# Kernel tuning notes

Hardware: AMD Instinct MI355X
Metric: run time of the kernel (lower is better)

## Reference

```python
import jax, jax.numpy as jnp
import numpy as np

ALPHA_LO = float(np.exp(-1.0 / 5.0))   # 0.81873...
ALPHA_HI = float(np.exp(-1.0 / 25.0))  # 0.96079...
T_CROP = 0


def setup_inputs() -> dict:
    key = jax.random.key(0)
    k1, k2, k3, k4 = jax.random.split(key, 4)
    B, T, I, H = 64, 2000, 512, 512
    x = jax.random.normal(k1, (B, T, I), dtype=jnp.float32)
    # W ~ U(-sqrt(1/I), sqrt(1/I)) per nn.init.uniform_
    lim = float(np.sqrt(1.0 / I))
    W = jax.random.uniform(k2, (H, I), dtype=jnp.float32, minval=-lim, maxval=lim)
    # alpha ~ U(alpha_lim[0], alpha_lim[1])
    alpha = jax.random.uniform(k3, (H,), dtype=jnp.float32, minval=ALPHA_LO, maxval=ALPHA_HI)
    # initial membrane potential ~ U(0,1) (torch.rand in _readout_cell)
    u0 = jax.random.uniform(k4, (B, H), dtype=jnp.float32)
    return {"x": x, "W": W, "alpha": alpha, "u0": u0}


def reference(x, W, alpha, u0):
    # x: [B, T, I], W: [H, I] -> Wx: [B, T, H]
    alpha_c = jnp.clip(alpha, ALPHA_LO, ALPHA_HI)  # [H]
    beta = 1.0 - alpha_c                           # [H]
    Wx = jnp.einsum("bti,hi->bth", x, W)          # [B, T, H]
    Wx_t = jnp.swapaxes(Wx, 0, 1)                  # [T, B, H] for scan

    out0 = jnp.zeros_like(u0)

    def step(carry, inp):
        ut, out, t = carry
        wx_t = inp  # [B, H]
        ut = alpha_c * ut + beta * wx_t
        out = out + jnp.where(t >= T_CROP, jax.nn.softmax(ut, axis=1), 0.0)
        return (ut, out, t + 1), None

    (_, out, _), _ = jax.lax.scan(step, (u0, out0, jnp.int32(0)), Wx_t)
    return out  # [B, H]
```

## Files before the change

kernel.cpp:

```cpp
#include <hip/hip_runtime.h>
#include <hip/hip_bf16.h>
#include <stdint.h>

#define ALPHA_LO 0.8187307530779818f
#define ALPHA_HI 0.9607894391523232f

#define BATCH 64
#define TT    2000
#define II    512
#define HH    512
#define MM    (BATCH*TT)
#define LCH   50
#define CCH   (TT/LCH)

typedef __bf16 bf16;
typedef bf16  bf16x8 __attribute__((ext_vector_type(8)));
typedef float f32x4  __attribute__((ext_vector_type(4)));

#define GLDS(src, dst) __builtin_amdgcn_global_load_lds( \
    (const __attribute__((address_space(1))) unsigned int*)(src), \
    (__attribute__((address_space(3))) unsigned int*)(dst), 16, 0, 0)

__global__ void k_convW(const float* __restrict__ W, bf16* __restrict__ Wbt) {
    const int t  = blockIdx.x * 256 + threadIdx.x;
    const int h  = t >> 6;
    const int kb = t & 63;
    const float* src = W + (size_t)h * II + kb * 8;
    float4 v0 = *(const float4*)(src);
    float4 v1 = *(const float4*)(src + 4);
    bf16x8 o;
    o[0]=(bf16)v0.x; o[1]=(bf16)v0.y; o[2]=(bf16)v0.z; o[3]=(bf16)v0.w;
    o[4]=(bf16)v1.x; o[5]=(bf16)v1.y; o[6]=(bf16)v1.z; o[7]=(bf16)v1.w;
    const int ks = kb >> 2, kq = kb & 3, jj = h >> 4, fr = h & 15;
    bf16* dst = Wbt + (size_t)ks * 16384 + jj * 512 + kq * 128 + fr * 8;
    *(bf16x8*)dst = o;
}

__global__ __launch_bounds__(256, 2) void k_gemm(const float* __restrict__ X,
                                                 const bf16* __restrict__ Wbt,
                                                 bf16* __restrict__ Y) {
    __shared__ bf16 Al[2][4096];
    __shared__ bf16 Bl[3][8192];
    const int tid  = threadIdx.x;
    const int swz  = (blockIdx.x & 7) * 250 + (blockIdx.x >> 3);
    const int m0   = (swz >> 1) * 128;
    const int nt   = swz & 1;
    const int lane = tid & 63;
    const int wv   = tid >> 6;
    const int wm   = wv >> 1;
    const int wn   = wv & 1;

    f32x4 acc[4][8] = {};

    const int fr0  = tid & 15;
    const int akq  = (tid >> 4) & 3;
    const int row0 = ((tid >> 6) << 4) + fr0;
    const float* xa = X + (size_t)(m0 + row0) * II + akq * 8;
    const int aoff = tid * 8;

    const bf16* bsrc = Wbt + nt * 8192 + lane * 8;

    float4 av[3][4];

    #pragma unroll
    for (int q = 0; q < 4; ++q) GLDS(bsrc + (q * 4 + wv) * 512,         &Bl[0][(q * 4 + wv) * 512]);
    av[0][0] = *(const float4*)(xa);
    av[0][1] = *(const float4*)(xa + 4);
    av[0][2] = *(const float4*)(xa + 32768);
    av[0][3] = *(const float4*)(xa + 32772);
    #pragma unroll
    for (int q = 0; q < 4; ++q) GLDS(bsrc + 16384 + (q * 4 + wv) * 512, &Bl[1][(q * 4 + wv) * 512]);
    av[1][0] = *(const float4*)(xa + 32);
    av[1][1] = *(const float4*)(xa + 36);
    av[1][2] = *(const float4*)(xa + 32800);
    av[1][3] = *(const float4*)(xa + 32804);

    #pragma unroll
    for (int ks = 0; ks < 16; ++ks) {
        const int bcur = ks % 3;
        const int acur = ks & 1;
        if (ks + 2 < 16) {
            const int nb = (ks + 2) % 3;
            #pragma unroll
            for (int q = 0; q < 4; ++q)
                GLDS(bsrc + (size_t)(ks + 2) * 16384 + (q * 4 + wv) * 512,
                     &Bl[nb][(q * 4 + wv) * 512]);
            av[nb][0] = *(const float4*)(xa + (size_t)(ks + 2) * 32);
            av[nb][1] = *(const float4*)(xa + (size_t)(ks + 2) * 32 + 4);
            av[nb][2] = *(const float4*)(xa + (size_t)(ks + 2) * 32 + 32768);
            av[nb][3] = *(const float4*)(xa + (size_t)(ks + 2) * 32 + 32772);
        }
        {
            float4 a0 = av[bcur][0], a1 = av[bcur][1];
            float4 a2 = av[bcur][2], a3 = av[bcur][3];
            bf16x8 c0, c1;
            c0[0]=(bf16)a0.x; c0[1]=(bf16)a0.y; c0[2]=(bf16)a0.z; c0[3]=(bf16)a0.w;
            c0[4]=(bf16)a1.x; c0[5]=(bf16)a1.y; c0[6]=(bf16)a1.z; c0[7]=(bf16)a1.w;
            c1[0]=(bf16)a2.x; c1[1]=(bf16)a2.y; c1[2]=(bf16)a2.z; c1[3]=(bf16)a2.w;
            c1[4]=(bf16)a3.x; c1[5]=(bf16)a3.y; c1[6]=(bf16)a3.z; c1[7]=(bf16)a3.w;
            *(bf16x8*)(&Al[acur][aoff])        = c0;
            *(bf16x8*)(&Al[acur][aoff + 2048]) = c1;
        }
        asm volatile("s_waitcnt lgkmcnt(0)" ::: "memory");
        __builtin_amdgcn_s_barrier();
        bf16x8 af[4], bb[8];
        #pragma unroll
        for (int i = 0; i < 4; ++i)
            af[i] = *(const bf16x8*)(&Al[acur][(wm * 4 + i) * 512 + lane * 8]);
        #pragma unroll
        for (int j = 0; j < 8; ++j)
            bb[j] = *(const bf16x8*)(&Bl[bcur][(wn * 8 + j) * 512 + lane * 8]);
        __builtin_amdgcn_s_setprio(1);
        #pragma unroll
        for (int i = 0; i < 4; ++i)
            #pragma unroll
            for (int j = 0; j < 8; ++j)
                acc[i][j] = __builtin_amdgcn_mfma_f32_16x16x32_bf16(af[i], bb[j], acc[i][j], 0, 0, 0);
        __builtin_amdgcn_s_setprio(0);
        asm volatile("" ::: "memory");
    }

    const int fr = lane & 15;
    const int kq = lane >> 4;
    #pragma unroll
    for (int i = 0; i < 4; ++i)
        #pragma unroll
        for (int j = 0; j < 8; ++j) {
            const int row = m0 + wm * 64 + i * 16 + kq * 4;
            const int col = nt * 256 + (wn * 8 + j) * 16 + fr;
            #pragma unroll
            for (int r = 0; r < 4; ++r)
                Y[(size_t)(row + r) * HH + col] = (bf16)acc[i][j][r];
        }
}

__global__ void k_chunk(const bf16* __restrict__ Y, const float* __restrict__ alpha,
                        float* __restrict__ P) {
    const int c = blockIdx.x, b = blockIdx.y;
    const int lane = threadIdx.x;
    const int h0 = lane * 8;
    float a[8], p[8];
    #pragma unroll
    for (int k = 0; k < 8; ++k) {
        a[k] = fminf(fmaxf(alpha[h0 + k], ALPHA_LO), ALPHA_HI);
        p[k] = 0.f;
    }
    const bf16* base = Y + ((size_t)b * TT + (size_t)c * LCH) * HH + h0;
    for (int j = 0; j < LCH; ++j) {
        bf16x8 w = *(const bf16x8*)(base + (size_t)j * HH);
        #pragma unroll
        for (int k = 0; k < 8; ++k) p[k] = a[k] * p[k] + (float)w[k];
    }
    float* po = P + ((size_t)c * BATCH + b) * HH + h0;
    #pragma unroll
    for (int k = 0; k < 8; ++k) po[k] = (1.f - a[k]) * p[k];
}

__global__ void k_prefix(const float* __restrict__ alpha, const float* __restrict__ u0,
                         const float* __restrict__ P, float* __restrict__ V) {
    const int g = blockIdx.x * 256 + threadIdx.x;
    const int h = g & (HH - 1);
    float a = fminf(fmaxf(alpha[h], ALPHA_LO), ALPHA_HI);
    float a2 = a * a, a4 = a2 * a2, a5 = a4 * a;
    float b2 = a5 * a5, b4 = b2 * b2, a25 = b4 * a5;
    float aL = a25 * a25;
    float v = u0[g];
    for (int c = 0; c < CCH; ++c) {
        const size_t idx = (size_t)c * (BATCH * HH) + g;
        V[idx] = v;
        v = aL * v + P[idx];
    }
}

__global__ void k_soft(const bf16* __restrict__ Y, const float* __restrict__ alpha,
                       const float* __restrict__ V, float* __restrict__ OutP) {
    const int c = blockIdx.x, b = blockIdx.y;
    const int lane = threadIdx.x;
    const int h0 = lane * 8;
    float a[8], bt[8], u[8], o[8];
    #pragma unroll
    for (int k = 0; k < 8; ++k) {
        a[k]  = fminf(fmaxf(alpha[h0 + k], ALPHA_LO), ALPHA_HI);
        bt[k] = 1.f - a[k];
        o[k]  = 0.f;
    }
    const float* vb = V + ((size_t)c * BATCH + b) * HH + h0;
    #pragma unroll
    for (int k = 0; k < 8; ++k) u[k] = vb[k];
    const bf16* base = Y + ((size_t)b * TT + (size_t)c * LCH) * HH + h0;
    for (int j = 0; j < LCH; ++j) {
        bf16x8 w = *(const bf16x8*)(base + (size_t)j * HH);
        float e[8], s = 0.f;
        #pragma unroll
        for (int k = 0; k < 8; ++k) {
            u[k] = a[k] * u[k] + bt[k] * (float)w[k];
            e[k] = __expf(u[k]);
            s += e[k];
        }
        #pragma unroll
        for (int off = 32; off >= 1; off >>= 1) s += __shfl_xor(s, off, 64);
        const float inv = 1.f / s;
        #pragma unroll
        for (int k = 0; k < 8; ++k) o[k] += e[k] * inv;
    }
    float* po = OutP + ((size_t)c * BATCH + b) * HH + h0;
    #pragma unroll
    for (int k = 0; k < 8; ++k) po[k] = o[k];
}

__global__ void k_reduce(const float* __restrict__ OutP, float* __restrict__ out) {
    const int g = blockIdx.x * 256 + threadIdx.x;
    float s = 0.f;
    for (int c = 0; c < CCH; ++c) s += OutP[(size_t)c * (BATCH * HH) + g];
    out[g] = s;
}

extern "C" void kernel_launch(void* const* d_in, const int* in_sizes, int n_in,
                              void* d_out, int out_size, void* d_ws, size_t ws_size,
                              hipStream_t stream) {
    const float* x     = (const float*)d_in[0];
    const float* W     = (const float*)d_in[1];
    const float* alpha = (const float*)d_in[2];
    const float* u0    = (const float*)d_in[3];
    float* out = (float*)d_out;

    char* ws = (char*)d_ws;
    bf16* Wbt = (bf16*)ws;
    bf16* Yx  = (bf16*)(ws + 524288);
    float* P  = (float*)(ws + 524288 + 131072000);
    float* V  = P + (size_t)CCH * BATCH * HH;
    float* OutP = V + (size_t)CCH * BATCH * HH;

    hipLaunchKernelGGL(k_convW,  dim3(128),          dim3(256), 0, stream, W, Wbt);
    hipLaunchKernelGGL(k_gemm,   dim3(2000),         dim3(256), 0, stream, x, Wbt, Yx);
    hipLaunchKernelGGL(k_chunk,  dim3(CCH, BATCH),   dim3(64),  0, stream, Yx, alpha, P);
    hipLaunchKernelGGL(k_prefix, dim3(BATCH*HH/256), dim3(256), 0, stream, alpha, u0, P, V);
    hipLaunchKernelGGL(k_soft,   dim3(CCH, BATCH),   dim3(64),  0, stream, Yx, alpha, V, OutP);
    hipLaunchKernelGGL(k_reduce, dim3(BATCH*HH/256), dim3(256), 0, stream, OutP, out);
}
```

Baseline: 213.3 us.

## Load GEMM operands directly from global into registers, dropping LDS staging

The GEMM kernel no longer stages A (converted fp32 rows) and B (bf16 weights) through shared memory with barriers. Each wave now loads its own A rows and B fragments straight from global memory into registers, double-buffering A one k-step ahead. This removes the LDS writes and reads and the per-step barrier, but each wave now fetches data that was previously shared across waves. That doubles the global and L2 traffic for A and B and shortens the prefetch distance for B.

```diff
diff --git a/kernel.cpp b/kernel.cpp
--- a/kernel.cpp
+++ b/kernel.cpp
@@ -16,10 +16,6 @@
 typedef __bf16 bf16;
 typedef bf16  bf16x8 __attribute__((ext_vector_type(8)));
 typedef float f32x4  __attribute__((ext_vector_type(4)));
-
-#define GLDS(src, dst) __builtin_amdgcn_global_load_lds( \
-    (const __attribute__((address_space(1))) unsigned int*)(src), \
-    (__attribute__((address_space(3))) unsigned int*)(dst), 16, 0, 0)
 
 __global__ void k_convW(const float* __restrict__ W, bf16* __restrict__ Wbt) {
     const int t  = blockIdx.x * 256 + threadIdx.x;
@@ -39,8 +35,6 @@
 __global__ __launch_bounds__(256, 2) void k_gemm(const float* __restrict__ X,
                                                  const bf16* __restrict__ Wbt,
                                                  bf16* __restrict__ Y) {
-    __shared__ bf16 Al[2][4096];
-    __shared__ bf16 Bl[3][8192];
     const int tid  = threadIdx.x;
     const int swz  = (blockIdx.x & 7) * 250 + (blockIdx.x >> 3);
     const int m0   = (swz >> 1) * 128;
@@ -49,67 +43,45 @@
     const int wv   = tid >> 6;
     const int wm   = wv >> 1;
     const int wn   = wv & 1;
+    const int fr   = lane & 15;
+    const int kq   = lane >> 4;
 
     f32x4 acc[4][8] = {};
 
-    const int fr0  = tid & 15;
-    const int akq  = (tid >> 4) & 3;
-    const int row0 = ((tid >> 6) << 4) + fr0;
-    const float* xa = X + (size_t)(m0 + row0) * II + akq * 8;
-    const int aoff = tid * 8;
-
-    const bf16* bsrc = Wbt + nt * 8192 + lane * 8;
-
-    float4 av[3][4];
-
-    #pragma unroll
-    for (int q = 0; q < 4; ++q) GLDS(bsrc + (q * 4 + wv) * 512,         &Bl[0][(q * 4 + wv) * 512]);
-    av[0][0] = *(const float4*)(xa);
-    av[0][1] = *(const float4*)(xa + 4);
-    av[0][2] = *(const float4*)(xa + 32768);
-    av[0][3] = *(const float4*)(xa + 32772);
-    #pragma unroll
-    for (int q = 0; q < 4; ++q) GLDS(bsrc + 16384 + (q * 4 + wv) * 512, &Bl[1][(q * 4 + wv) * 512]);
-    av[1][0] = *(const float4*)(xa + 32);
-    av[1][1] = *(const float4*)(xa + 36);
-    av[1][2] = *(const float4*)(xa + 32800);
-    av[1][3] = *(const float4*)(xa + 32804);
+    const float* abase[4];
+    #pragma unroll
+    for (int i = 0; i < 4; ++i)
+        abase[i] = X + (size_t)(m0 + wm * 64 + i * 16 + fr) * II + kq * 8;
+
+    const bf16* bbase = Wbt + (size_t)(nt * 16 + wn * 8) * 512 + lane * 8;
+
+    float4 avb[2][4][2];
+    #pragma unroll
+    for (int i = 0; i < 4; ++i) {
+        avb[0][i][0] = *(const float4*)(abase[i]);
+        avb[0][i][1] = *(const float4*)(abase[i] + 4);
+    }
 
     #pragma unroll
     for (int ks = 0; ks < 16; ++ks) {
-        const int bcur = ks % 3;
-        const int acur = ks & 1;
-        if (ks + 2 < 16) {
-            const int nb = (ks + 2) % 3;
+        bf16x8 bb[8];
+        #pragma unroll
+        for (int j = 0; j < 8; ++j)
+            bb[j] = *(const bf16x8*)(bbase + (size_t)ks * 16384 + j * 512);
+        bf16x8 af[4];
+        #pragma unroll
+        for (int i = 0; i < 4; ++i) {
+            float4 a0 = avb[ks & 1][i][0], a1 = avb[ks & 1][i][1];
+            af[i][0]=(bf16)a0.x; af[i][1]=(bf16)a0.y; af[i][2]=(bf16)a0.z; af[i][3]=(bf16)a0.w;
+            af[i][4]=(bf16)a1.x; af[i][5]=(bf16)a1.y; af[i][6]=(bf16)a1.z; af[i][7]=(bf16)a1.w;
+        }
+        if (ks < 15) {
             #pragma unroll
-            for (int q = 0; q < 4; ++q)
-                GLDS(bsrc + (size_t)(ks + 2) * 16384 + (q * 4 + wv) * 512,
-                     &Bl[nb][(q * 4 + wv) * 512]);
-            av[nb][0] = *(const float4*)(xa + (size_t)(ks + 2) * 32);
-            av[nb][1] = *(const float4*)(xa + (size_t)(ks + 2) * 32 + 4);
-            av[nb][2] = *(const float4*)(xa + (size_t)(ks + 2) * 32 + 32768);
-            av[nb][3] = *(const float4*)(xa + (size_t)(ks + 2) * 32 + 32772);
-        }
-        {
-            float4 a0 = av[bcur][0], a1 = av[bcur][1];
-            float4 a2 = av[bcur][2], a3 = av[bcur][3];
-            bf16x8 c0, c1;
-            c0[0]=(bf16)a0.x; c0[1]=(bf16)a0.y; c0[2]=(bf16)a0.z; c0[3]=(bf16)a0.w;
-            c0[4]=(bf16)a1.x; c0[5]=(bf16)a1.y; c0[6]=(bf16)a1.z; c0[7]=(bf16)a1.w;
-            c1[0]=(bf16)a2.x; c1[1]=(bf16)a2.y; c1[2]=(bf16)a2.z; c1[3]=(bf16)a2.w;
-            c1[4]=(bf16)a3.x; c1[5]=(bf16)a3.y; c1[6]=(bf16)a3.z; c1[7]=(bf16)a3.w;
-            *(bf16x8*)(&Al[acur][aoff])        = c0;
-            *(bf16x8*)(&Al[acur][aoff + 2048]) = c1;
-        }
-        asm volatile("s_waitcnt lgkmcnt(0)" ::: "memory");
-        __builtin_amdgcn_s_barrier();
-        bf16x8 af[4], bb[8];
-        #pragma unroll
-        for (int i = 0; i < 4; ++i)
-            af[i] = *(const bf16x8*)(&Al[acur][(wm * 4 + i) * 512 + lane * 8]);
-        #pragma unroll
-        for (int j = 0; j < 8; ++j)
-            bb[j] = *(const bf16x8*)(&Bl[bcur][(wn * 8 + j) * 512 + lane * 8]);
+            for (int i = 0; i < 4; ++i) {
+                avb[(ks + 1) & 1][i][0] = *(const float4*)(abase[i] + (ks + 1) * 32);
+                avb[(ks + 1) & 1][i][1] = *(const float4*)(abase[i] + (ks + 1) * 32 + 4);
+            }
+        }
         __builtin_amdgcn_s_setprio(1);
         #pragma unroll
         for (int i = 0; i < 4; ++i)
@@ -117,11 +89,8 @@
             for (int j = 0; j < 8; ++j)
                 acc[i][j] = __builtin_amdgcn_mfma_f32_16x16x32_bf16(af[i], bb[j], acc[i][j], 0, 0, 0);
         __builtin_amdgcn_s_setprio(0);
-        asm volatile("" ::: "memory");
-    }
-
-    const int fr = lane & 15;
-    const int kq = lane >> 4;
+    }
+
     #pragma unroll
     for (int i = 0; i < 4; ++i)
         #pragma unroll
```

After: 275.0 us. 29.0% more time.
